# Kernel tuning notes

Hardware: AMD Instinct MI355X
Metric: run time of the kernel (lower is better)

The kernel has to match this reference:

```python
import jax, jax.numpy as jnp
import numpy as np

DIVERSITY_WEIGHT = 0.3
UNCERTAINTY_WEIGHT = 0.3
EPS_NORM = 1e-12  # torch F.normalize eps
EPS_LOG = 1e-8


def setup_inputs() -> dict:
    key = jax.random.key(0)
    k1, k2 = jax.random.split(key)
    B, N, D, C = 8, 8192, 512, 2
    x = jax.random.normal(k1, (B, N, D), dtype=jnp.float32)
    c = jax.random.normal(k2, (B, N, C), dtype=jnp.float32)
    return {"x": x, "c": c, "big_lambda": 512}


def reference(x, c, big_lambda):
    B, N, D = x.shape
    C = c.shape[-1]
    big_lambda = min(big_lambda, N)

    # relevance: max class score per instance (C > 1 branch)
    if C == 1:
        relevance = c[..., 0]
    else:
        relevance = jnp.max(c, axis=-1)  # [B, N]

    # diversity: 1 - mean cosine similarity to all other patches.
    # Row-sum of the N x N cosine-sim matrix factorizes:
    #   sum_j xn_i . xn_j = xn_i . (sum_j xn_j)  -> O(N*D) instead of O(N^2*D)
    norms = jnp.linalg.norm(x, axis=-1, keepdims=True)
    x_norm = x / jnp.maximum(norms, EPS_NORM)          # [B, N, D]
    s = jnp.sum(x_norm, axis=1)                        # [B, D]
    row_sums = jnp.einsum('bnd,bd->bn', x_norm, s)     # [B, N]
    avg_sim = (row_sums - 1.0) / (N - 1)
    diversity = 1.0 - avg_sim

    # uncertainty: entropy of class distribution
    if C == 1:
        p = jax.nn.sigmoid(c[..., 0])
        probs = jnp.stack([1.0 - p, p], axis=-1)
    else:
        probs = jax.nn.softmax(c, axis=-1)
    uncertainty = -jnp.sum(probs * jnp.log(probs + EPS_LOG), axis=-1)  # [B, N]

    combined = relevance + DIVERSITY_WEIGHT * diversity + UNCERTAINTY_WEIGHT * uncertainty

    _, selected_indices = jax.lax.top_k(combined, big_lambda)  # [B, big_lambda]
    attention_weights = jax.nn.softmax(combined, axis=1)       # [B, N]
    return selected_indices, attention_weights
```

## Files before the change

kernel.cpp:

```cpp
#include <hip/hip_runtime.h>
#include <stdint.h>

#define B 8
#define N 8192
#define D 512
#define C 2
#define K 512
#define DIV_W 0.3f
#define UNC_W 0.3f

constexpr int ROWS_PER_WAVE  = 16;
constexpr int WAVES_PER_BLK  = 4;
constexpr int ROWS_PER_BLOCK = ROWS_PER_WAVE * WAVES_PER_BLK;
constexpr int BLOCKS_PER_B   = N / ROWS_PER_BLOCK;

__device__ __forceinline__ uint32_t ordmap(float f) {
    uint32_t u = __float_as_uint(f);
    return (u & 0x80000000u) ? ~u : (u | 0x80000000u);
}
__device__ __forceinline__ float ordunmap(uint32_t u) {
    return (u >> 31) ? __uint_as_float(u & 0x7FFFFFFFu) : __uint_as_float(~u);
}

__global__ __launch_bounds__(256) void k_norm_s(const float* __restrict__ x,
                                                float* __restrict__ inv_norm,
                                                float* __restrict__ partials) {
    int blk  = blockIdx.x;
    int b    = blk / BLOCKS_PER_B;
    int rb   = (blk % BLOCKS_PER_B) * ROWS_PER_BLOCK;
    int tid  = threadIdx.x;
    int wave = tid >> 6;
    int lane = tid & 63;

    const float4* xb = (const float4*)(x + (size_t)b * N * D);

    float4 accA = {0.f, 0.f, 0.f, 0.f};
    float4 accB = {0.f, 0.f, 0.f, 0.f};

    int row0 = rb + wave * ROWS_PER_WAVE;
    for (int r = 0; r < ROWS_PER_WAVE; ++r) {
        int row = row0 + r;
        const float4* xr = xb + (size_t)row * (D / 4);
        float4 a  = xr[lane];
        float4 bb = xr[64 + lane];

        float ss = a.x*a.x + a.y*a.y + a.z*a.z + a.w*a.w
                 + bb.x*bb.x + bb.y*bb.y + bb.z*bb.z + bb.w*bb.w;
        #pragma unroll
        for (int o = 32; o > 0; o >>= 1) ss += __shfl_xor(ss, o, 64);

        float inv = 1.0f / fmaxf(sqrtf(ss), 1e-12f);
        if (lane == 0) inv_norm[b * N + row] = inv;

        accA.x += a.x * inv;  accA.y += a.y * inv;
        accA.z += a.z * inv;  accA.w += a.w * inv;
        accB.x += bb.x * inv; accB.y += bb.y * inv;
        accB.z += bb.z * inv; accB.w += bb.w * inv;
    }

    __shared__ float sp[WAVES_PER_BLK][D];
    float* dA = &sp[wave][lane * 4];
    dA[0] = accA.x; dA[1] = accA.y; dA[2] = accA.z; dA[3] = accA.w;
    float* dB = &sp[wave][256 + lane * 4];
    dB[0] = accB.x; dB[1] = accB.y; dB[2] = accB.z; dB[3] = accB.w;
    __syncthreads();

    float* dst = partials + (size_t)blk * D;
    for (int d = tid; d < D; d += 256)
        dst[d] = sp[0][d] + sp[1][d] + sp[2][d] + sp[3][d];
}

__global__ __launch_bounds__(512) void k_reduce_s(const float* __restrict__ partials,
                                                  float* __restrict__ s) {
    int b = blockIdx.x;
    int d = threadIdx.x;
    const float* p = partials + (size_t)b * BLOCKS_PER_B * D + d;
    float acc = 0.f;
    #pragma unroll 8
    for (int j = 0; j < BLOCKS_PER_B; ++j) acc += p[(size_t)j * D];
    s[b * D + d] = acc;
}

__global__ __launch_bounds__(256) void k_combined(const float* __restrict__ x,
                                                  const float* __restrict__ c,
                                                  const float* __restrict__ inv_norm,
                                                  const float* __restrict__ s,
                                                  float* __restrict__ combined) {
    __shared__ float sl[D];
    int blk  = blockIdx.x;
    int b    = blk / BLOCKS_PER_B;
    int rb   = (blk % BLOCKS_PER_B) * ROWS_PER_BLOCK;
    int tid  = threadIdx.x;
    int wave = tid >> 6;
    int lane = tid & 63;

    for (int d = tid; d < D; d += 256) sl[d] = s[b * D + d];
    __syncthreads();

    const float4* sv = (const float4*)sl;
    float4 sA = sv[lane];
    float4 sB = sv[64 + lane];

    const float4* xb = (const float4*)(x + (size_t)b * N * D);
    int row0 = rb + wave * ROWS_PER_WAVE;
    for (int r = 0; r < ROWS_PER_WAVE; ++r) {
        int row = row0 + r;
        const float4* xr = xb + (size_t)row * (D / 4);
        float4 a  = xr[lane];
        float4 bb = xr[64 + lane];

        float dot = a.x*sA.x + a.y*sA.y + a.z*sA.z + a.w*sA.w
                  + bb.x*sB.x + bb.y*sB.y + bb.z*sB.z + bb.w*sB.w;
        #pragma unroll
        for (int o = 32; o > 0; o >>= 1) dot += __shfl_xor(dot, o, 64);

        if (lane == 0) {
            float rs  = dot * inv_norm[b * N + row];
            float div = 1.0f - (rs - 1.0f) / (float)(N - 1);

            const float* cc = c + ((size_t)b * N + row) * C;
            float c0 = cc[0], c1 = cc[1];
            float rel = fmaxf(c0, c1);
            float e0 = expf(c0 - rel), e1 = expf(c1 - rel);
            float Z  = e0 + e1;
            float p0 = e0 / Z, p1 = e1 / Z;
            float ent = -(p0 * logf(p0 + 1e-8f) + p1 * logf(p1 + 1e-8f));

            combined[b * N + row] = rel + DIV_W * div + UNC_W * ent;
        }
    }
}

__global__ __launch_bounds__(1024) void k_topk_sm(const float* __restrict__ combined,
                                                  float* __restrict__ out_idx,
                                                  float* __restrict__ out_w) {
    __shared__ uint64_t cand[K];
    __shared__ uint32_t hist[256];
    __shared__ uint32_t tiew[256];
    __shared__ uint32_t wred[16];
    __shared__ float    fred[16];
    __shared__ uint32_t sc_prefix, sc_remK, sc_cnt;

    const int b    = blockIdx.x;
    const int tid  = threadIdx.x;
    const int lane = tid & 63;
    const int wave = tid >> 6;

    const float4* cb4 = (const float4*)(combined + b * N);
    float4 f0 = cb4[tid];
    float4 f1 = cb4[1024 + tid];

    uint32_t v[8];
    v[0] = ordmap(f0.x); v[1] = ordmap(f0.y); v[2] = ordmap(f0.z); v[3] = ordmap(f0.w);
    v[4] = ordmap(f1.x); v[5] = ordmap(f1.y); v[6] = ordmap(f1.z); v[7] = ordmap(f1.w);

    uint32_t umax = 0;
    #pragma unroll
    for (int q = 0; q < 8; ++q) umax = max(umax, v[q]);
    #pragma unroll
    for (int o = 32; o > 0; o >>= 1) umax = max(umax, __shfl_xor(umax, o, 64));
    if (lane == 0) wred[wave] = umax;
    if (tid == 0) { sc_remK = K; sc_prefix = 0u; sc_cnt = 0u; }
    __syncthreads();
    uint32_t bmax = wred[0];
    #pragma unroll
    for (int q = 1; q < 16; ++q) bmax = max(bmax, wred[q]);
    const float m = ordunmap(bmax);

    float e[8];
    float sum = 0.f;
    #pragma unroll
    for (int q = 0; q < 8; ++q) { e[q] = expf(ordunmap(v[q]) - m); sum += e[q]; }
    #pragma unroll
    for (int o = 32; o > 0; o >>= 1) sum += __shfl_xor(sum, o, 64);
    if (lane == 0) fred[wave] = sum;
    __syncthreads();
    float Z = 0.f;
    #pragma unroll
    for (int q = 0; q < 16; ++q) Z += fred[q];
    const float invZ = 1.0f / Z;
    float4* ow = (float4*)(out_w + b * N);
    float4 w0 = {e[0]*invZ, e[1]*invZ, e[2]*invZ, e[3]*invZ};
    float4 w1 = {e[4]*invZ, e[5]*invZ, e[6]*invZ, e[7]*invZ};
    ow[tid]        = w0;
    ow[1024 + tid] = w1;

    uint32_t prefix = 0, maskHi = 0;
    for (int p = 3; p >= 0; --p) {
        if (tid < 256) hist[tid] = 0u;
        __syncthreads();
        const int sh = 8 * p;
        #pragma unroll
        for (int q = 0; q < 8; ++q) {
            if ((v[q] & maskHi) == prefix)
                atomicAdd(&hist[(v[q] >> sh) & 0xFFu], 1u);
        }
        __syncthreads();
        if (wave == 0) {
            uint32_t cc[4], lsum = 0;
            #pragma unroll
            for (int q = 0; q < 4; ++q) { cc[q] = hist[lane * 4 + q]; lsum += cc[q]; }
            uint32_t ssum = lsum;
            #pragma unroll
            for (int off = 1; off < 64; off <<= 1) {
                uint32_t t2 = __shfl_down(ssum, off, 64);
                if (lane + off < 64) ssum += t2;
            }
            uint32_t cum = ssum - lsum;
            const uint32_t remK = sc_remK;
            #pragma unroll
            for (int q = 3; q >= 0; --q) {
                if (cum < remK && cum + cc[q] >= remK) {
                    sc_prefix = prefix | ((uint32_t)(lane * 4 + q) << sh);
                    sc_remK   = remK - cum;
                }
                cum += cc[q];
            }
        }
        __syncthreads();
        prefix = sc_prefix;
        maskHi |= (0xFFu << sh);
    }
    const uint32_t T    = prefix;
    const uint32_t remF = sc_remK;

    if (tid < 256) tiew[tid] = 0u;
    __syncthreads();
    #pragma unroll
    for (int q = 0; q < 8; ++q) {
        uint32_t idx = (q < 4) ? (uint32_t)(4 * tid + q)
                               : (uint32_t)(4096 + 4 * tid + (q - 4));
        if (v[q] > T) {
            uint32_t slot = atomicAdd(&sc_cnt, 1u);
            cand[slot] = ((uint64_t)v[q] << 13) | (uint32_t)(8191 - idx);
        } else if (v[q] == T) {
            atomicOr(&tiew[idx >> 5], 1u << (idx & 31));
        }
    }
    __syncthreads();
    const uint32_t base = sc_cnt;
    if (wave == 0) {
        const int w0i = lane * 4;
        uint32_t lsum = 0;
        #pragma unroll
        for (int q = 0; q < 4; ++q) lsum += __popc(tiew[w0i + q]);
        uint32_t ssum = lsum;
        #pragma unroll
        for (int off = 1; off < 64; off <<= 1) {
            uint32_t t2 = __shfl_up(ssum, off, 64);
            if (lane >= off) ssum += t2;
        }
        uint32_t rank = ssum - lsum;
        for (int q = 0; q < 4; ++q) {
            uint32_t word = tiew[w0i + q];
            while (word) {
                int bpos = __builtin_ctz(word);
                if (rank < remF) {
                    uint32_t idx = (uint32_t)(w0i + q) * 32u + (uint32_t)bpos;
                    cand[base + rank] = ((uint64_t)T << 13) | (uint32_t)(8191 - idx);
                }
                rank++;
                word &= word - 1;
            }
        }
    }
    __syncthreads();

    uint64_t sv = (tid < K) ? cand[tid] : 0ULL;
    __syncthreads();
    for (int k = 2; k <= K; k <<= 1) {
        for (int j = k >> 1; j > 0; j >>= 1) {
            const bool desc  = ((tid & k) == 0);
            const bool lower = ((tid & j) == 0);
            uint64_t pv;
            if (j >= 64) {
                if (tid < K) cand[tid] = sv;
                __syncthreads();
                pv = (tid < K) ? cand[tid ^ j] : 0ULL;
                __syncthreads();
            } else {
                pv = __shfl_xor(sv, j, 64);
            }
            const bool keepmax = (lower == desc);
            if (tid < K && (keepmax ? (pv > sv) : (pv < sv))) sv = pv;
        }
    }
    if (tid < K)
        out_idx[b * K + tid] = (float)(8191u - (uint32_t)(sv & 0x1FFFu));
}

extern "C" void kernel_launch(void* const* d_in, const int* in_sizes, int n_in,
                              void* d_out, int out_size, void* d_ws, size_t ws_size,
                              hipStream_t stream) {
    const float* x = (const float*)d_in[0];
    const float* c = (const float*)d_in[1];

    float* ws       = (float*)d_ws;
    float* partials = ws;
    float* s        = partials + B * BLOCKS_PER_B * D;
    float* inv_norm = s + B * D;
    float* combined = inv_norm + B * N;

    float* out = (float*)d_out;

    k_norm_s  <<<B * BLOCKS_PER_B, 256, 0, stream>>>(x, inv_norm, partials);
    k_reduce_s<<<B, 512, 0, stream>>>(partials, s);
    k_combined<<<B * BLOCKS_PER_B, 256, 0, stream>>>(x, c, inv_norm, s, combined);
    k_topk_sm <<<B, 1024, 0, stream>>>(combined, out, out + B * K);
}
```

Measured before the change: 78.43 us.

## Move relevance/entropy into norm pass, aggregate top-k atomics per wave

The per-row relevance and entropy terms, plus the constant part of diversity, are now computed in the first norm kernel. The combined kernel only subtracts the dot-product term, so it reads the partial value back instead of loading c. In top-k, the first radix histogram pass uses wave-level match-and-count to cut LDS atomic contention, and candidate compaction uses ballot-based per-wave slot reservation. The reduce unroll factor is also raised. This adds a read-modify-write of combined and extra ballot loops in exchange for fewer serialized atomics and less serial lane-0 work.

```diff
diff --git a/kernel.cpp b/kernel.cpp
--- a/kernel.cpp
+++ b/kernel.cpp
@@ -4,7 +4,6 @@
 #define B 8
 #define N 8192
 #define D 512
-#define C 2
 #define K 512
 #define DIV_W 0.3f
 #define UNC_W 0.3f
@@ -14,6 +13,9 @@
 constexpr int ROWS_PER_BLOCK = ROWS_PER_WAVE * WAVES_PER_BLK;
 constexpr int BLOCKS_PER_B   = N / ROWS_PER_BLOCK;
 
+constexpr float DIVC = DIV_W * (1.0f + 1.0f / 8191.0f);
+constexpr float COEF = DIV_W / 8191.0f;
+
 __device__ __forceinline__ uint32_t ordmap(float f) {
     uint32_t u = __float_as_uint(f);
     return (u & 0x80000000u) ? ~u : (u | 0x80000000u);
@@ -23,8 +25,10 @@
 }
 
 __global__ __launch_bounds__(256) void k_norm_s(const float* __restrict__ x,
+                                                const float* __restrict__ c,
                                                 float* __restrict__ inv_norm,
-                                                float* __restrict__ partials) {
+                                                float* __restrict__ partials,
+                                                float* __restrict__ combined) {
     int blk  = blockIdx.x;
     int b    = blk / BLOCKS_PER_B;
     int rb   = (blk % BLOCKS_PER_B) * ROWS_PER_BLOCK;
@@ -58,6 +62,17 @@
         accB.z += bb.z * inv; accB.w += bb.w * inv;
     }
 
+    if (lane < 16) {
+        int row = row0 + lane;
+        float2 cv = ((const float2*)(c))[(size_t)b * N + row];
+        float rel = fmaxf(cv.x, cv.y);
+        float e0 = expf(cv.x - rel), e1 = expf(cv.y - rel);
+        float Z  = e0 + e1;
+        float p0 = e0 / Z, p1 = e1 / Z;
+        float ent = -(p0 * logf(p0 + 1e-8f) + p1 * logf(p1 + 1e-8f));
+        combined[b * N + row] = rel + UNC_W * ent + DIVC;
+    }
+
     __shared__ float sp[WAVES_PER_BLK][D];
     float* dA = &sp[wave][lane * 4];
     dA[0] = accA.x; dA[1] = accA.y; dA[2] = accA.z; dA[3] = accA.w;
@@ -76,13 +91,12 @@
     int d = threadIdx.x;
     const float* p = partials + (size_t)b * BLOCKS_PER_B * D + d;
     float acc = 0.f;
-    #pragma unroll 8
+    #pragma unroll 16
     for (int j = 0; j < BLOCKS_PER_B; ++j) acc += p[(size_t)j * D];
     s[b * D + d] = acc;
 }
 
 __global__ __launch_bounds__(256) void k_combined(const float* __restrict__ x,
-                                                  const float* __restrict__ c,
                                                   const float* __restrict__ inv_norm,
                                                   const float* __restrict__ s,
                                                   float* __restrict__ combined) {
@@ -115,18 +129,8 @@
         for (int o = 32; o > 0; o >>= 1) dot += __shfl_xor(dot, o, 64);
 
         if (lane == 0) {
-            float rs  = dot * inv_norm[b * N + row];
-            float div = 1.0f - (rs - 1.0f) / (float)(N - 1);
-
-            const float* cc = c + ((size_t)b * N + row) * C;
-            float c0 = cc[0], c1 = cc[1];
-            float rel = fmaxf(c0, c1);
-            float e0 = expf(c0 - rel), e1 = expf(c1 - rel);
-            float Z  = e0 + e1;
-            float p0 = e0 / Z, p1 = e1 / Z;
-            float ent = -(p0 * logf(p0 + 1e-8f) + p1 * logf(p1 + 1e-8f));
-
-            combined[b * N + row] = rel + DIV_W * div + UNC_W * ent;
+            float rs = dot * inv_norm[b * N + row];
+            combined[b * N + row] = combined[b * N + row] - COEF * rs;
         }
     }
 }
@@ -190,10 +194,27 @@
         if (tid < 256) hist[tid] = 0u;
         __syncthreads();
         const int sh = 8 * p;
-        #pragma unroll
-        for (int q = 0; q < 8; ++q) {
-            if ((v[q] & maskHi) == prefix)
-                atomicAdd(&hist[(v[q] >> sh) & 0xFFu], 1u);
+        if (p == 3) {
+            #pragma unroll
+            for (int q = 0; q < 8; ++q) {
+                uint32_t bin = v[q] >> 24;
+                bool pred = true;
+                unsigned long long todo = ~0ULL;
+                while (todo) {
+                    int leader = __ffsll(todo) - 1;
+                    uint32_t lbin = __shfl(bin, leader, 64);
+                    unsigned long long same = __ballot(pred && (bin == lbin));
+                    if (lane == leader) atomicAdd(&hist[lbin], (uint32_t)__popcll(same));
+                    todo &= ~same;
+                    if (bin == lbin) pred = false;
+                }
+            }
+        } else {
+            #pragma unroll
+            for (int q = 0; q < 8; ++q) {
+                if ((v[q] & maskHi) == prefix)
+                    atomicAdd(&hist[(v[q] >> sh) & 0xFFu], 1u);
+            }
         }
         __syncthreads();
         if (wave == 0) {
@@ -230,12 +251,20 @@
     for (int q = 0; q < 8; ++q) {
         uint32_t idx = (q < 4) ? (uint32_t)(4 * tid + q)
                                : (uint32_t)(4096 + 4 * tid + (q - 4));
-        if (v[q] > T) {
-            uint32_t slot = atomicAdd(&sc_cnt, 1u);
-            cand[slot] = ((uint64_t)v[q] << 13) | (uint32_t)(8191 - idx);
-        } else if (v[q] == T) {
-            atomicOr(&tiew[idx >> 5], 1u << (idx & 31));
-        }
+        bool g = (v[q] > T);
+        unsigned long long mask = __ballot(g);
+        if (mask) {
+            int leader = __ffsll(mask) - 1;
+            uint32_t bcnt = (uint32_t)__popcll(mask);
+            uint32_t wbase = 0;
+            if (lane == leader) wbase = atomicAdd(&sc_cnt, bcnt);
+            wbase = __shfl(wbase, leader, 64);
+            if (g) {
+                uint32_t off = (uint32_t)__popcll(mask & ((1ULL << lane) - 1ULL));
+                cand[wbase + off] = ((uint64_t)v[q] << 13) | (uint32_t)(8191 - idx);
+            }
+        }
+        if (v[q] == T) atomicOr(&tiew[idx >> 5], 1u << (idx & 31));
     }
     __syncthreads();
     const uint32_t base = sc_cnt;
@@ -303,8 +332,8 @@
 
     float* out = (float*)d_out;
 
-    k_norm_s  <<<B * BLOCKS_PER_B, 256, 0, stream>>>(x, inv_norm, partials);
+    k_norm_s  <<<B * BLOCKS_PER_B, 256, 0, stream>>>(x, c, inv_norm, partials, combined);
     k_reduce_s<<<B, 512, 0, stream>>>(partials, s);
-    k_combined<<<B * BLOCKS_PER_B, 256, 0, stream>>>(x, c, inv_norm, s, combined);
+    k_combined<<<B * BLOCKS_PER_B, 256, 0, stream>>>(x, inv_norm, s, combined);
     k_topk_sm <<<B, 1024, 0, stream>>>(combined, out, out + B * K);
 }
```

After: 81.14 us. +3.5%, slower.
